# Optimization experiments

Measured on AMD Instinct MI355X. Metric: run time of the kernel, lower is better.

## Reference

```python
import jax, jax.numpy as jnp
import numpy as np

HID = 256


def _mlp(h, ws, bs):
    # 4-layer MLP: tanh x3, sigmoid output (matches nn.Sequential in torch code)
    h = jnp.tanh(h @ ws[0] + bs[0])
    h = jnp.tanh(h @ ws[1] + bs[1])
    h = jnp.tanh(h @ ws[2] + bs[2])
    return jax.nn.sigmoid(h @ ws[3] + bs[3])


def setup_inputs() -> dict:
    key = jax.random.key(0)
    N, K, DE = 100000, 32, 8
    IN1 = K * DE          # 256
    MID = 5
    IN2 = K * MID         # 160
    E = N * K
    ks = jax.random.split(key, 20)
    x = jax.random.normal(ks[0], (N, DE), dtype=jnp.float32)
    edge_index = jax.random.randint(ks[1], (2, E), 0, N, dtype=jnp.int64)
    edge_attr = jax.random.normal(ks[2], (E, DE), dtype=jnp.float32)

    def lin(k, fan_in, fan_out):
        kw, kb = jax.random.split(k)
        lim = 1.0 / np.sqrt(fan_in)
        w = jax.random.uniform(kw, (fan_in, fan_out), jnp.float32, -lim, lim)
        b = jax.random.uniform(kb, (fan_out,), jnp.float32, -lim, lim)
        return w, b

    dims1 = [(IN1, HID), (HID, HID), (HID, HID), (HID, MID)]
    dims2 = [(IN2, HID), (HID, HID), (HID, HID), (HID, 1)]
    inp = {"x": x, "edge_index": edge_index, "edge_attr": edge_attr}
    for i, (fi, fo) in enumerate(dims1):
        w, b = lin(ks[3 + i], fi, fo)
        inp[f"w1_{i}"], inp[f"b1_{i}"] = w, b
    for i, (fi, fo) in enumerate(dims2):
        w, b = lin(ks[10 + i], fi, fo)
        inp[f"w2_{i}"], inp[f"b2_{i}"] = w, b
    return inp


def reference(x, edge_index, edge_attr,
              w1_0, b1_0, w1_1, b1_1, w1_2, b1_2, w1_3, b1_3,
              w2_0, b2_0, w2_1, b2_1, w2_2, b2_2, w2_3, b2_3):
    K = 32
    IN1 = w1_0.shape[0]              # 256
    MID = w1_3.shape[1]              # 5
    # GNN1: message = edge_attr; aggregate reshapes to [N, IN1] then MLP -> [N, MID]
    out1 = _mlp(edge_attr.reshape(-1, IN1), (w1_0, w1_1, w1_2, w1_3), (b1_0, b1_1, b1_2, b1_3))
    # GNN2: message = x_j = out1[edge_index[1]] (flow='target_to_source')
    gathered = out1[edge_index[1]]                     # [E, MID] irregular gather
    out2 = _mlp(gathered.reshape(-1, K * MID), (w2_0, w2_1, w2_2, w2_3), (b2_0, b2_1, b2_2, b2_3))
    return out2[:, 0]                                  # squeeze dim 1 -> [N]
```

## Files before the change

kernel.cpp:

```cpp
#include <hip/hip_runtime.h>
#include <stdint.h>

typedef uint16_t u16;
typedef uint32_t u32;
typedef __attribute__((ext_vector_type(8)))  __bf16 bf16x8;
typedef __attribute__((ext_vector_type(16))) float  f32x16;
typedef __attribute__((ext_vector_type(4)))  float  f32x4;
typedef __attribute__((ext_vector_type(2)))  u32    u32x2;

#define NROWS   100000
#define E_EDGES 3200000

#define HIDX(r, g) (((r) << 8) + ((((g) ^ ((r) & 31))) << 3))

#define MFMA(a, b, c) __builtin_amdgcn_mfma_f32_32x32x16_bf16((a), (b), (c), 0, 0, 0)

__device__ __forceinline__ u32 bfpack(float a, float b) {
    u16 lo = __builtin_bit_cast(u16, (__bf16)a);
    u16 hi = __builtin_bit_cast(u16, (__bf16)b);
    return (u32)lo | ((u32)hi << 16);
}
__device__ __forceinline__ float fast_tanh(float x) {
    float e = __builtin_amdgcn_exp2f(x * 2.885390081777927f);
    float r = __builtin_amdgcn_rcpf(e + 1.0f);
    return __builtin_fmaf(-2.0f, r, 1.0f);
}
__device__ __forceinline__ float fast_sigmoid(float x) {
    float e = __builtin_amdgcn_exp2f(x * -1.4426950408889634f);
    return __builtin_amdgcn_rcpf(1.0f + e);
}

__device__ __forceinline__ void dense256(u16* __restrict__ Hs, const u16* __restrict__ WB,
                                         const float* __restrict__ bias,
                                         int wave, int l31, int lh) {
    f32x16 acc[4];
#pragma unroll
    for (int i = 0; i < 4; ++i)
#pragma unroll
        for (int j = 0; j < 16; ++j) acc[i][j] = 0.0f;

    const u16* wp = WB + wave * 16384 + l31 * 16 + lh * 8;
    bf16x8 wq0[3], wq1[3];
#pragma unroll
    for (int d = 0; d < 3; ++d) {
        wq0[d] = *(const bf16x8*)(wp + d * 512);
        wq1[d] = *(const bf16x8*)(wp + 8192 + d * 512);
    }

    __syncthreads();

    bf16x8 hq0[2], hq1[2];
#pragma unroll
    for (int d = 0; d < 2; ++d) {
        const int g = 2 * d + lh;
        hq0[d] = *(const bf16x8*)(Hs + HIDX(l31, g));
        hq1[d] = *(const bf16x8*)(Hs + HIDX(32 + l31, g));
    }

#pragma unroll
    for (int s = 0; s < 16; ++s) {
        const int cw = s % 3, ch = s & 1;
        bf16x8 w0 = wq0[cw], w1 = wq1[cw], h0 = hq0[ch], h1 = hq1[ch];
        if (s + 3 < 16) {
            wq0[cw] = *(const bf16x8*)(wp + (s + 3) * 512);
            wq1[cw] = *(const bf16x8*)(wp + 8192 + (s + 3) * 512);
        }
        if (s + 2 < 16) {
            const int ng = 2 * (s + 2) + lh;
            hq0[ch] = *(const bf16x8*)(Hs + HIDX(l31, ng));
            hq1[ch] = *(const bf16x8*)(Hs + HIDX(32 + l31, ng));
        }
        acc[0] = MFMA(w0, h0, acc[0]);
        acc[1] = MFMA(w0, h1, acc[1]);
        acc[2] = MFMA(w1, h0, acc[2]);
        acc[3] = MFMA(w1, h1, acc[3]);
    }
    __syncthreads();

#pragma unroll
    for (int i = 0; i < 2; ++i) {
        const int nt = wave * 2 + i;
#pragma unroll
        for (int rg = 0; rg < 4; ++rg) {
            const float4 bv = *(const float4*)(bias + nt * 32 + rg * 8 + lh * 4);
#pragma unroll
            for (int b = 0; b < 2; ++b) {
                const f32x16& A = acc[i * 2 + b];
                float x0 = fast_tanh(A[rg * 4 + 0] + bv.x);
                float x1 = fast_tanh(A[rg * 4 + 1] + bv.y);
                float x2 = fast_tanh(A[rg * 4 + 2] + bv.z);
                float x3 = fast_tanh(A[rg * 4 + 3] + bv.w);
                const int r = b * 32 + l31;
                const int g = nt * 4 + rg;
                uint2 v; v.x = bfpack(x0, x1); v.y = bfpack(x2, x3);
                *(uint2*)(Hs + (r << 8) + (((g) ^ (r & 31)) << 3) + lh * 4) = v;
            }
        }
    }
}

__device__ __forceinline__ f32x16 final_dense(const u16* __restrict__ Hs,
                                              const u16* __restrict__ WBf,
                                              int wave, int l31, int lh) {
    __syncthreads();
    f32x16 acc;
#pragma unroll
    for (int j = 0; j < 16; ++j) acc[j] = 0.0f;
    if (wave < 2) {
        const u16* wp = WBf + l31 * 16 + lh * 8;
        bf16x8 wq[2], hq[2];
#pragma unroll
        for (int d = 0; d < 2; ++d) {
            wq[d] = *(const bf16x8*)(wp + d * 512);
            hq[d] = *(const bf16x8*)(Hs + HIDX(wave * 32 + l31, 2 * d + lh));
        }
#pragma unroll
        for (int s = 0; s < 16; ++s) {
            const int c = s & 1;
            bf16x8 w = wq[c], h = hq[c];
            if (s + 2 < 16) {
                wq[c] = *(const bf16x8*)(wp + (s + 2) * 512);
                hq[c] = *(const bf16x8*)(Hs + HIDX(wave * 32 + l31, 2 * (s + 2) + lh));
            }
            acc = MFMA(w, h, acc);
        }
    }
    return acc;
}

__global__ __launch_bounds__(256, 4) void mlp1_kernel(
    const float* __restrict__ ea, const u16* __restrict__ WB1, const u16* __restrict__ WB13,
    const float* __restrict__ b0, const float* __restrict__ b1, const float* __restrict__ b2,
    const float* __restrict__ b3, u16* __restrict__ out1) {
    __shared__ u16 Hs[64 * 256];
    const int tid = threadIdx.x, wave = tid >> 6, lane = tid & 63, blk = blockIdx.x;
    const int l31 = lane & 31, lh = lane >> 5;

#pragma unroll
    for (int i = 0; i < 8; ++i) {
        const int li = i * 256 + tid;
        const int r = li >> 5, g = li & 31;
        const int rg_ = blk * 64 + r;
        uint4 v = {0u, 0u, 0u, 0u};
        if (rg_ < NROWS) {
            const float* p = ea + (size_t)rg_ * 256 + g * 8;
            f32x4 a0 = __builtin_nontemporal_load((const f32x4*)p);
            f32x4 a1 = __builtin_nontemporal_load((const f32x4*)p + 1);
            v.x = bfpack(a0.x, a0.y); v.y = bfpack(a0.z, a0.w);
            v.z = bfpack(a1.x, a1.y); v.w = bfpack(a1.z, a1.w);
        }
        *(uint4*)(Hs + HIDX(r, g)) = v;
    }
    dense256(Hs, WB1,          b0, wave, l31, lh);
    dense256(Hs, WB1 + 65536,  b1, wave, l31, lh);
    dense256(Hs, WB1 + 131072, b2, wave, l31, lh);
    f32x16 acc = final_dense(Hs, WB13, wave, l31, lh);

    if (wave < 2) {
        const int row_g = blk * 64 + wave * 32 + l31;
        if (row_g < NROWS) {
            if (lh == 0) {
                float s0 = fast_sigmoid(acc[0] + b3[0]);
                float s1 = fast_sigmoid(acc[1] + b3[1]);
                float s2 = fast_sigmoid(acc[2] + b3[2]);
                float s3 = fast_sigmoid(acc[3] + b3[3]);
                u32x2 v; v.x = bfpack(s0, s1); v.y = bfpack(s2, s3);
                __builtin_nontemporal_store(v, (u32x2*)(out1 + (size_t)row_g * 8));
            } else {
                float s4 = fast_sigmoid(acc[0] + b3[4]);
                u32x2 v; v.x = bfpack(s4, 0.0f); v.y = 0u;
                __builtin_nontemporal_store(v, (u32x2*)(out1 + (size_t)row_g * 8 + 4));
            }
        }
    }
}

__global__ __launch_bounds__(256, 4) void mlp2_kernel(
    const int* __restrict__ idx1, const u16* __restrict__ out1,
    const u16* __restrict__ WB2, const u16* __restrict__ WB23,
    const float* __restrict__ b0, const float* __restrict__ b1, const float* __restrict__ b2,
    const float* __restrict__ b3, float* __restrict__ out) {
    __shared__ u16 Hs[64 * 256];
    const int tid = threadIdx.x, wave = tid >> 6, lane = tid & 63, blk = blockIdx.x;
    const int l31 = lane & 31, lh = lane >> 5;

    int nodes[8];
#pragma unroll
    for (int i = 0; i < 8; ++i) {
        const long e = (long)blk * 2048 + i * 256 + tid;
        nodes[i] = (e < (long)E_EDGES) ? __builtin_nontemporal_load(idx1 + e) : -1;
    }
#pragma unroll
    for (int i = 0; i < 8; ++i) {
        const int li = i * 256 + tid;
        const int r = li >> 5, j = li & 31;
        uint4 v = {0u, 0u, 0u, 0u};
        if (nodes[i] >= 0) v = *(const uint4*)(out1 + (size_t)nodes[i] * 8);
        *(uint4*)(Hs + HIDX(r, j)) = v;
    }
    dense256(Hs, WB2,          b0, wave, l31, lh);
    dense256(Hs, WB2 + 65536,  b1, wave, l31, lh);
    dense256(Hs, WB2 + 131072, b2, wave, l31, lh);
    f32x16 acc = final_dense(Hs, WB23, wave, l31, lh);

    if (wave < 2) {
        const int row_g = blk * 64 + wave * 32 + l31;
        if (row_g < NROWS && lh == 0)
            __builtin_nontemporal_store(fast_sigmoid(acc[0] + b3[0]), out + row_g);
    }
}

__global__ void transform_kernel(
    const float* __restrict__ w10, const float* __restrict__ w11, const float* __restrict__ w12,
    const float* __restrict__ w13, const float* __restrict__ w20, const float* __restrict__ w21,
    const float* __restrict__ w22, const float* __restrict__ w23, u16* __restrict__ ws) {
    const int id = blockIdx.x * 256 + threadIdx.x;
    float val;
    if (id < 196608) {
        int layer = id >> 16, id2 = id & 65535;
        int nw = id2 >> 14, t = (id2 >> 13) & 1, s = (id2 >> 9) & 15;
        int l31 = (id2 >> 4) & 31, lhe = id2 & 15;
        int n = ((nw << 1) | t) * 32 + l31;
        int k = s * 16 + lhe;
        const float* w = layer == 0 ? w10 : (layer == 1 ? w11 : w12);
        val = w[k * 256 + n];
    } else if (id < 204800) {
        int rem = id - 196608;
        int s = rem >> 9, n = (rem >> 4) & 31, kl = rem & 15;
        int k = s * 16 + kl;
        val = (n < 5) ? w13[k * 5 + n] : 0.0f;
    } else if (id < 401408) {
        int rem = id - 204800;
        int layer = rem >> 16, id2 = rem & 65535;
        int nw = id2 >> 14, t = (id2 >> 13) & 1, s = (id2 >> 9) & 15;
        int l31 = (id2 >> 4) & 31, lhe = id2 & 15;
        int n = ((nw << 1) | t) * 32 + l31;
        int k = s * 16 + lhe;
        if (layer == 0) {
            int j = k >> 3, v = k & 7;
            val = (v < 5) ? w20[(j * 5 + v) * 256 + n] : 0.0f;
        } else {
            val = (layer == 1 ? w21 : w22)[k * 256 + n];
        }
    } else {
        int rem = id - 401408;
        int s = rem >> 9, n = (rem >> 4) & 31, kl = rem & 15;
        int k = s * 16 + kl;
        val = (n == 0) ? w23[k] : 0.0f;
    }
    u32 u = __builtin_bit_cast(u32, val);
    u = (u + 0x7FFFu + ((u >> 16) & 1u)) >> 16;
    ws[id] = (u16)u;
}

extern "C" void kernel_launch(void* const* d_in, const int* in_sizes, int n_in,
                              void* d_out, int out_size, void* d_ws, size_t ws_size,
                              hipStream_t stream) {
    const int*   ei  = (const int*)d_in[1];
    const float* ea  = (const float*)d_in[2];
    const float* w10 = (const float*)d_in[3];  const float* b10 = (const float*)d_in[4];
    const float* w11 = (const float*)d_in[5];  const float* b11 = (const float*)d_in[6];
    const float* w12 = (const float*)d_in[7];  const float* b12 = (const float*)d_in[8];
    const float* w13 = (const float*)d_in[9];  const float* b13 = (const float*)d_in[10];
    const float* w20 = (const float*)d_in[11]; const float* b20 = (const float*)d_in[12];
    const float* w21 = (const float*)d_in[13]; const float* b21 = (const float*)d_in[14];
    const float* w22 = (const float*)d_in[15]; const float* b22 = (const float*)d_in[16];
    const float* w23 = (const float*)d_in[17]; const float* b23 = (const float*)d_in[18];

    u16* ws   = (u16*)d_ws;
    u16* WB1  = ws;
    u16* WB13 = ws + 196608;
    u16* WB2  = ws + 204800;
    u16* WB23 = ws + 401408;
    u16* out1 = ws + 409600;

    hipLaunchKernelGGL(transform_kernel, dim3(1600), dim3(256), 0, stream,
                       w10, w11, w12, w13, w20, w21, w22, w23, ws);
    hipLaunchKernelGGL(mlp1_kernel, dim3(1563), dim3(256), 0, stream,
                       ea, WB1, WB13, b10, b11, b12, b13, out1);
    hipLaunchKernelGGL(mlp2_kernel, dim3(1563), dim3(256), 0, stream,
                       ei + E_EDGES, out1, WB2, WB23, b20, b21, b22, b23, (float*)d_out);
}
```

Baseline: 319.3 us.

## Make MLP kernels persistent with an atomic tile work queue

Both MLP kernels now launch a fixed grid of 1024 blocks, matching 4 blocks per CU on 256 CUs. Each block loops over 64-row tiles and fetches its next tile index from a global atomic counter. The counters are initialised in the transform kernel, and out1 is shifted in the workspace to make room for them. The aim is to remove the partial second wave and tail imbalance of the 1563-block launch. In exchange it adds one atomic and one block-wide barrier per tile.

```diff
diff --git a/kernel.cpp b/kernel.cpp
--- a/kernel.cpp
+++ b/kernel.cpp
@@ -10,6 +10,8 @@
 
 #define NROWS   100000
 #define E_EDGES 3200000
+#define NTILES  1563
+#define GRID    1024
 
 #define HIDX(r, g) (((r) << 8) + ((((g) ^ ((r) & 31))) << 3))
 
@@ -131,47 +133,54 @@
 __global__ __launch_bounds__(256, 4) void mlp1_kernel(
     const float* __restrict__ ea, const u16* __restrict__ WB1, const u16* __restrict__ WB13,
     const float* __restrict__ b0, const float* __restrict__ b1, const float* __restrict__ b2,
-    const float* __restrict__ b3, u16* __restrict__ out1) {
+    const float* __restrict__ b3, u16* __restrict__ out1, u32* __restrict__ cnt) {
     __shared__ u16 Hs[64 * 256];
-    const int tid = threadIdx.x, wave = tid >> 6, lane = tid & 63, blk = blockIdx.x;
+    __shared__ int tshare;
+    const int tid = threadIdx.x, wave = tid >> 6, lane = tid & 63;
     const int l31 = lane & 31, lh = lane >> 5;
 
-#pragma unroll
-    for (int i = 0; i < 8; ++i) {
-        const int li = i * 256 + tid;
-        const int r = li >> 5, g = li & 31;
-        const int rg_ = blk * 64 + r;
-        uint4 v = {0u, 0u, 0u, 0u};
-        if (rg_ < NROWS) {
-            const float* p = ea + (size_t)rg_ * 256 + g * 8;
-            f32x4 a0 = __builtin_nontemporal_load((const f32x4*)p);
-            f32x4 a1 = __builtin_nontemporal_load((const f32x4*)p + 1);
-            v.x = bfpack(a0.x, a0.y); v.y = bfpack(a0.z, a0.w);
-            v.z = bfpack(a1.x, a1.y); v.w = bfpack(a1.z, a1.w);
-        }
-        *(uint4*)(Hs + HIDX(r, g)) = v;
-    }
-    dense256(Hs, WB1,          b0, wave, l31, lh);
-    dense256(Hs, WB1 + 65536,  b1, wave, l31, lh);
-    dense256(Hs, WB1 + 131072, b2, wave, l31, lh);
-    f32x16 acc = final_dense(Hs, WB13, wave, l31, lh);
-
-    if (wave < 2) {
-        const int row_g = blk * 64 + wave * 32 + l31;
-        if (row_g < NROWS) {
-            if (lh == 0) {
-                float s0 = fast_sigmoid(acc[0] + b3[0]);
-                float s1 = fast_sigmoid(acc[1] + b3[1]);
-                float s2 = fast_sigmoid(acc[2] + b3[2]);
-                float s3 = fast_sigmoid(acc[3] + b3[3]);
-                u32x2 v; v.x = bfpack(s0, s1); v.y = bfpack(s2, s3);
-                __builtin_nontemporal_store(v, (u32x2*)(out1 + (size_t)row_g * 8));
-            } else {
-                float s4 = fast_sigmoid(acc[0] + b3[4]);
-                u32x2 v; v.x = bfpack(s4, 0.0f); v.y = 0u;
-                __builtin_nontemporal_store(v, (u32x2*)(out1 + (size_t)row_g * 8 + 4));
+    int t = blockIdx.x;
+    while (t < NTILES) {
+#pragma unroll
+        for (int i = 0; i < 8; ++i) {
+            const int li = i * 256 + tid;
+            const int r = li >> 5, g = li & 31;
+            const int rg_ = t * 64 + r;
+            uint4 v = {0u, 0u, 0u, 0u};
+            if (rg_ < NROWS) {
+                const float* p = ea + (size_t)rg_ * 256 + g * 8;
+                f32x4 a0 = __builtin_nontemporal_load((const f32x4*)p);
+                f32x4 a1 = __builtin_nontemporal_load((const f32x4*)p + 1);
+                v.x = bfpack(a0.x, a0.y); v.y = bfpack(a0.z, a0.w);
+                v.z = bfpack(a1.x, a1.y); v.w = bfpack(a1.z, a1.w);
             }
-        }
+            *(uint4*)(Hs + HIDX(r, g)) = v;
+        }
+        dense256(Hs, WB1,          b0, wave, l31, lh);
+        dense256(Hs, WB1 + 65536,  b1, wave, l31, lh);
+        dense256(Hs, WB1 + 131072, b2, wave, l31, lh);
+        f32x16 acc = final_dense(Hs, WB13, wave, l31, lh);
+
+        if (wave < 2) {
+            const int row_g = t * 64 + wave * 32 + l31;
+            if (row_g < NROWS) {
+                if (lh == 0) {
+                    float s0 = fast_sigmoid(acc[0] + b3[0]);
+                    float s1 = fast_sigmoid(acc[1] + b3[1]);
+                    float s2 = fast_sigmoid(acc[2] + b3[2]);
+                    float s3 = fast_sigmoid(acc[3] + b3[3]);
+                    u32x2 v; v.x = bfpack(s0, s1); v.y = bfpack(s2, s3);
+                    __builtin_nontemporal_store(v, (u32x2*)(out1 + (size_t)row_g * 8));
+                } else {
+                    float s4 = fast_sigmoid(acc[0] + b3[4]);
+                    u32x2 v; v.x = bfpack(s4, 0.0f); v.y = 0u;
+                    __builtin_nontemporal_store(v, (u32x2*)(out1 + (size_t)row_g * 8 + 4));
+                }
+            }
+        }
+        if (tid == 0) tshare = (int)atomicAdd(cnt, 1u);
+        __syncthreads();
+        t = tshare;
     }
 }
 
@@ -179,34 +188,41 @@
     const int* __restrict__ idx1, const u16* __restrict__ out1,
     const u16* __restrict__ WB2, const u16* __restrict__ WB23,
     const float* __restrict__ b0, const float* __restrict__ b1, const float* __restrict__ b2,
-    const float* __restrict__ b3, float* __restrict__ out) {
+    const float* __restrict__ b3, float* __restrict__ out, u32* __restrict__ cnt) {
     __shared__ u16 Hs[64 * 256];
-    const int tid = threadIdx.x, wave = tid >> 6, lane = tid & 63, blk = blockIdx.x;
+    __shared__ int tshare;
+    const int tid = threadIdx.x, wave = tid >> 6, lane = tid & 63;
     const int l31 = lane & 31, lh = lane >> 5;
 
-    int nodes[8];
-#pragma unroll
-    for (int i = 0; i < 8; ++i) {
-        const long e = (long)blk * 2048 + i * 256 + tid;
-        nodes[i] = (e < (long)E_EDGES) ? __builtin_nontemporal_load(idx1 + e) : -1;
-    }
-#pragma unroll
-    for (int i = 0; i < 8; ++i) {
-        const int li = i * 256 + tid;
-        const int r = li >> 5, j = li & 31;
-        uint4 v = {0u, 0u, 0u, 0u};
-        if (nodes[i] >= 0) v = *(const uint4*)(out1 + (size_t)nodes[i] * 8);
-        *(uint4*)(Hs + HIDX(r, j)) = v;
-    }
-    dense256(Hs, WB2,          b0, wave, l31, lh);
-    dense256(Hs, WB2 + 65536,  b1, wave, l31, lh);
-    dense256(Hs, WB2 + 131072, b2, wave, l31, lh);
-    f32x16 acc = final_dense(Hs, WB23, wave, l31, lh);
-
-    if (wave < 2) {
-        const int row_g = blk * 64 + wave * 32 + l31;
-        if (row_g < NROWS && lh == 0)
-            __builtin_nontemporal_store(fast_sigmoid(acc[0] + b3[0]), out + row_g);
+    int t = blockIdx.x;
+    while (t < NTILES) {
+        int nodes[8];
+#pragma unroll
+        for (int i = 0; i < 8; ++i) {
+            const long e = (long)t * 2048 + i * 256 + tid;
+            nodes[i] = (e < (long)E_EDGES) ? __builtin_nontemporal_load(idx1 + e) : -1;
+        }
+#pragma unroll
+        for (int i = 0; i < 8; ++i) {
+            const int li = i * 256 + tid;
+            const int r = li >> 5, j = li & 31;
+            uint4 v = {0u, 0u, 0u, 0u};
+            if (nodes[i] >= 0) v = *(const uint4*)(out1 + (size_t)nodes[i] * 8);
+            *(uint4*)(Hs + HIDX(r, j)) = v;
+        }
+        dense256(Hs, WB2,          b0, wave, l31, lh);
+        dense256(Hs, WB2 + 65536,  b1, wave, l31, lh);
+        dense256(Hs, WB2 + 131072, b2, wave, l31, lh);
+        f32x16 acc = final_dense(Hs, WB23, wave, l31, lh);
+
+        if (wave < 2) {
+            const int row_g = t * 64 + wave * 32 + l31;
+            if (row_g < NROWS && lh == 0)
+                __builtin_nontemporal_store(fast_sigmoid(acc[0] + b3[0]), out + row_g);
+        }
+        if (tid == 0) tshare = (int)atomicAdd(cnt, 1u);
+        __syncthreads();
+        t = tshare;
     }
 }
 
@@ -215,6 +231,10 @@
     const float* __restrict__ w13, const float* __restrict__ w20, const float* __restrict__ w21,
     const float* __restrict__ w22, const float* __restrict__ w23, u16* __restrict__ ws) {
     const int id = blockIdx.x * 256 + threadIdx.x;
+    if (id == 0) {
+        u32* cnt = (u32*)(ws + 409600);
+        cnt[0] = GRID; cnt[1] = GRID;
+    }
     float val;
     if (id < 196608) {
         int layer = id >> 16, id2 = id & 65535;
@@ -272,12 +292,14 @@
     u16* WB13 = ws + 196608;
     u16* WB2  = ws + 204800;
     u16* WB23 = ws + 401408;
-    u16* out1 = ws + 409600;
+    u32* cnt  = (u32*)(ws + 409600);
+    u16* out1 = ws + 409608;
 
     hipLaunchKernelGGL(transform_kernel, dim3(1600), dim3(256), 0, stream,
                        w10, w11, w12, w13, w20, w21, w22, w23, ws);
-    hipLaunchKernelGGL(mlp1_kernel, dim3(1563), dim3(256), 0, stream,
-                       ea, WB1, WB13, b10, b11, b12, b13, out1);
-    hipLaunchKernelGGL(mlp2_kernel, dim3(1563), dim3(256), 0, stream,
-                       ei + E_EDGES, out1, WB2, WB23, b20, b21, b22, b23, (float*)d_out);
-}
+    hipLaunchKernelGGL(mlp1_kernel, dim3(GRID), dim3(256), 0, stream,
+                       ea, WB1, WB13, b10, b11, b12, b13, out1, cnt + 0);
+    hipLaunchKernelGGL(mlp2_kernel, dim3(GRID), dim3(256), 0, stream,
+                       ei + E_EDGES, out1, WB2, WB23, b20, b21, b22, b23, (float*)d_out,
+                       cnt + 1);
+}
```

New measurement: 984.0 us. +208.2%, slower.
